# Optimization experiments

Measured on AMD Instinct MI355X. Metric: run time of the kernel, lower is better.

## Reference

```python
import jax, jax.numpy as jnp
import numpy as np

N = 20000      # nodes (human PPI network scale)
E = 640000     # edges (avg degree 32)
PE, GOS, PROT = 128, 128, 480
OM_DIMS = [3, 3, 24, 24]          # transcriptome, proteome, effectome, interactome
D = 384                           # latent_space_dimension = 128 * 3 (jk 'cat')
H = 128                           # hidden_channels per layer
NEG_SLOPE = 0.1


def setup_inputs() -> dict:
    key = jax.random.key(0)
    ks = jax.random.split(key, 64)
    rn = lambda k, shp, s=0.05: jax.random.normal(k, shp, jnp.float32) * s
    inp = {
        "x": jax.random.normal(ks[0], (N, PE + GOS + PROT), jnp.float32),
        "x_ft": jax.random.normal(ks[1], (N, sum(OM_DIMS)), jnp.float32),
        "edge_index": jax.random.randint(ks[2], (2, E), 0, N),
    }
    i = 3
    def lin(fin, fout, name):
        nonlocal i
        inp["W_" + name] = rn(ks[i], (fin, fout)); inp["b_" + name] = jnp.zeros((fout,), jnp.float32)
        i += 1
    lin(PE, D, "pe"); lin(GOS, D, "gos"); lin(PROT, D, "prot")
    for j, d in enumerate(OM_DIMS):
        lin(d, D, f"om{j}")
    dims = [D, H, H, H]
    for j in range(3):
        lin(dims[j], dims[j + 1], f"c{j}")   # feature-branch GCN convs
        lin(dims[j], dims[j + 1], f"o{j}")   # omics-branch GCN convs
    lin(2 * D, D, "lat")
    lin(D, H, "drug"); lin(D, H, "dis")
    lin(H, 2, "odrug"); lin(H, 2, "odis")
    return inp


def _gcn(x, W, b, src, dst, deg_inv):
    # GCNConv(improved=True): A_hat = A + 2I, sym norm D^-1/2 A_hat D^-1/2
    h = x @ W                                  # [N, F_out]
    coef = deg_inv[src] * deg_inv[dst]         # [E]
    agg = jax.ops.segment_sum(h[src] * coef[:, None], dst, num_segments=N)
    agg = agg + h * (2.0 * deg_inv * deg_inv)[:, None]   # self loops (weight 2)
    return agg + b


def reference(x, x_ft, edge_index,
              W_pe, b_pe, W_gos, b_gos, W_prot, b_prot,
              W_om0, b_om0, W_om1, b_om1, W_om2, b_om2, W_om3, b_om3,
              W_c0, b_c0, W_o0, b_o0, W_c1, b_c1, W_o1, b_o1, W_c2, b_c2, W_o2, b_o2,
              W_lat, b_lat, W_drug, b_drug, W_dis, b_dis,
              W_odrug, b_odrug, W_odis, b_odis):
    act = lambda t: jax.nn.leaky_relu(t, NEG_SLOPE)
    src, dst = edge_index[0], edge_index[1]
    deg = jax.ops.segment_sum(jnp.ones((E,), jnp.float32), dst, num_segments=N) + 2.0
    deg_inv = jax.lax.rsqrt(deg)

    # encoders (features branch): pe | gosemsim | prot_emb slices of x
    pe = x[:, :PE]; gos = x[:, PE:PE + GOS]; prot = x[:, PE + GOS:PE + GOS + PROT]
    h = act(pe @ W_pe + b_pe + gos @ W_gos + b_gos + prot @ W_prot + b_prot)

    # encoders (omics branch): 3|3|24|24 slices of x_ft
    offs = np.cumsum([0] + OM_DIMS)
    Wom = [W_om0, W_om1, W_om2, W_om3]; bom = [b_om0, b_om1, b_om2, b_om3]
    g = act(sum(x_ft[:, offs[j]:offs[j + 1]] @ Wom[j] + bom[j] for j in range(4)))

    Wc = [W_c0, W_c1, W_c2]; bc = [b_c0, b_c1, b_c2]
    Wo = [W_o0, W_o1, W_o2]; bo = [b_o0, b_o1, b_o2]
    hs, gs = [], []
    for j in range(3):
        h = act(_gcn(h, Wc[j], bc[j], src, dst, deg_inv)); hs.append(h)
        g = act(_gcn(g, Wo[j], bo[j], src, dst, deg_inv)); gs.append(g)
    jk = jnp.concatenate(hs, axis=-1)          # [N, 384]
    jk_om = jnp.concatenate(gs, axis=-1)       # [N, 384]

    z = act(jnp.concatenate([jk, jk_om], axis=-1) @ W_lat + b_lat)  # [N, 384]
    drug = act(z @ W_drug + b_drug) @ W_odrug + b_odrug             # [N, 2]
    dis = act(z @ W_dis + b_dis) @ W_odis + b_odis                  # [N, 2]
    return jnp.concatenate([drug, dis], axis=-1)                    # [N, 4]
```

## Files before the change

### kernel.cpp

```cpp
#include <hip/hip_runtime.h>
#include <cstdint>

#define NN 20000
#define NNP 20096
#define NE 640000
#define NEG_SLOPE 0.1f
#define NSCAN 79
#define NSL 8
#define NPSL 2500
#define FBPS 160

typedef unsigned short ushort_t;
typedef __attribute__((ext_vector_type(8))) short short8;
typedef __attribute__((ext_vector_type(4))) float f32x4;
typedef __attribute__((ext_vector_type(2))) float f32x2;

__device__ __forceinline__ unsigned short f2bf(float f) {
    union { float f; unsigned u; } v; v.f = f;
    unsigned r = v.u + 0x7fffu + ((v.u >> 16) & 1u);
    return (unsigned short)(r >> 16);
}
__device__ __forceinline__ float bflo(unsigned u) { return __uint_as_float(u << 16); }
__device__ __forceinline__ float bfhi(unsigned u) { return __uint_as_float(u & 0xffff0000u); }

__device__ __forceinline__ int swz(int r) { return (r ^ (r >> 2)) & 3; }

__device__ __forceinline__ void gld_lds16(const void* g, void* l) {
    __builtin_amdgcn_global_load_lds(
        (const __attribute__((address_space(1))) void*)g,
        (__attribute__((address_space(3))) void*)l,
        16, 0, 0);
}

#define O_CAT   0
#define O_OM    282624
#define O_C0    307200
#define O_O0    356352
#define O_C1    405504
#define O_O1    421888
#define O_C2    438272
#define O_O2    454656
#define O_LAT   471040
#define O_HEADS 765952
#define WT_TOTAL 864256

__global__ __launch_bounds__(256) void pack_weights(
    const float* __restrict__ Wpe, const float* __restrict__ Wgos, const float* __restrict__ Wprot,
    const float* __restrict__ bpe, const float* __restrict__ bgos, const float* __restrict__ bprot,
    const float* __restrict__ Wom0, const float* __restrict__ Wom1,
    const float* __restrict__ Wom2, const float* __restrict__ Wom3,
    const float* __restrict__ bom0, const float* __restrict__ bom1,
    const float* __restrict__ bom2, const float* __restrict__ bom3,
    const float* __restrict__ Wc0, const float* __restrict__ Wo0,
    const float* __restrict__ Wc1, const float* __restrict__ Wo1,
    const float* __restrict__ Wc2, const float* __restrict__ Wo2,
    const float* __restrict__ Wlat,
    const float* __restrict__ Wdrug, const float* __restrict__ Wdis,
    const float* __restrict__ bdrug, const float* __restrict__ bdis,
    ushort_t* __restrict__ Wt, float* __restrict__ bcat, float* __restrict__ bomc,
    float* __restrict__ bheads)
{
    int i = blockIdx.x * blockDim.x + threadIdx.x;
    if (i < 282624) {
        int m = i / 736, k = i % 736;
        float v = (k < 128) ? Wpe[k * 384 + m]
                : (k < 256) ? Wgos[(k - 128) * 384 + m]
                            : Wprot[(k - 256) * 384 + m];
        Wt[O_CAT + i] = f2bf(v);
        return;
    }
    i -= 282624;
    if (i < 24576) {
        int m = i / 64, k = i % 64;
        float v = (k < 3)  ? Wom0[k * 384 + m]
                : (k < 6)  ? Wom1[(k - 3) * 384 + m]
                : (k < 30) ? Wom2[(k - 6) * 384 + m]
                : (k < 54) ? Wom3[(k - 30) * 384 + m] : 0.f;
        Wt[O_OM + i] = f2bf(v);
        return;
    }
    i -= 24576;
    if (i < 49152) { int m = i / 384, k = i % 384; Wt[O_C0 + i] = f2bf(Wc0[k * 128 + m]); return; }
    i -= 49152;
    if (i < 49152) { int m = i / 384, k = i % 384; Wt[O_O0 + i] = f2bf(Wo0[k * 128 + m]); return; }
    i -= 49152;
    if (i < 16384) { int m = i / 128, k = i % 128; Wt[O_C1 + i] = f2bf(Wc1[k * 128 + m]); return; }
    i -= 16384;
    if (i < 16384) { int m = i / 128, k = i % 128; Wt[O_O1 + i] = f2bf(Wo1[k * 128 + m]); return; }
    i -= 16384;
    if (i < 16384) { int m = i / 128, k = i % 128; Wt[O_C2 + i] = f2bf(Wc2[k * 128 + m]); return; }
    i -= 16384;
    if (i < 16384) { int m = i / 128, k = i % 128; Wt[O_O2 + i] = f2bf(Wo2[k * 128 + m]); return; }
    i -= 16384;
    if (i < 294912) { int m = i / 768, k = i % 768; Wt[O_LAT + i] = f2bf(Wlat[k * 384 + m]); return; }
    i -= 294912;
    if (i < 98304) {
        int m = i / 384, k = i % 384;
        float v = (m < 128) ? Wdrug[k * 128 + m] : Wdis[k * 128 + (m - 128)];
        Wt[O_HEADS + i] = f2bf(v);
        return;
    }
    i -= 98304;
    if (i < 384) { bcat[i] = bpe[i] + bgos[i] + bprot[i]; return; }
    i -= 384;
    if (i < 384) { bomc[i] = bom0[i] + bom1[i] + bom2[i] + bom3[i]; return; }
    i -= 384;
    if (i < 256) { bheads[i] = (i < 128) ? bdrug[i] : bdis[i - 128]; return; }
}

#define CVT_T1 (NN * 736 / 4)
__global__ __launch_bounds__(256) void convert_inputs(
    const float* __restrict__ x, const float* __restrict__ xft,
    ushort_t* __restrict__ xb, ushort_t* __restrict__ xftb)
{
    int i = blockIdx.x * blockDim.x + threadIdx.x;
    if (i < CVT_T1) {
        int base = i * 4;
        float4 v = *reinterpret_cast<const float4*>(&x[base]);
        unsigned long long p = (unsigned long long)f2bf(v.x)
                             | ((unsigned long long)f2bf(v.y) << 16)
                             | ((unsigned long long)f2bf(v.z) << 32)
                             | ((unsigned long long)f2bf(v.w) << 48);
        *reinterpret_cast<unsigned long long*>(&xb[base]) = p;
        return;
    }
    i -= CVT_T1;
    if (i < NN * 64) {
        int r = i >> 6, c = i & 63;
        float v = (c < 54) ? xft[r * 54 + c] : 0.f;
        xftb[i] = f2bf(v);
    }
}

__global__ __launch_bounds__(256) void count_deg_sliced(const int* __restrict__ dst, int* __restrict__ cnt)
{
    const int slice = blockIdx.x & (NSL - 1);
    const int blk = blockIdx.x >> 3;
    const int lo = slice * NPSL, hi = lo + NPSL;
    for (int e = blk * 256 + threadIdx.x; e < NE; e += FBPS * 256) {
        int d = dst[e];
        if (d >= lo && d < hi) atomicAdd(&cnt[d], 1);
    }
}

__global__ __launch_bounds__(256) void scan_blocksums(const int* __restrict__ cnt, int* __restrict__ bsum,
                                                      float* __restrict__ deg_inv)
{
    __shared__ int s[256];
    int t = threadIdx.x, i = blockIdx.x * 256 + t;
    int v = (i < NN) ? cnt[i] : 0;
    if (i < NN) deg_inv[i] = rsqrtf((float)v + 2.0f);
    s[t] = v;
    __syncthreads();
    for (int off = 128; off; off >>= 1) {
        if (t < off) s[t] += s[t + off];
        __syncthreads();
    }
    if (t == 0) bsum[blockIdx.x] = s[0];
}

__global__ __launch_bounds__(128) void scan_tops(const int* __restrict__ bsum,
                                                 int* __restrict__ boff, int* __restrict__ ofs)
{
    __shared__ int s[NSCAN];
    int t = threadIdx.x;
    if (t < NSCAN) s[t] = bsum[t];
    __syncthreads();
    if (t == 0) {
        int run = 0;
        for (int b = 0; b < NSCAN; b++) { int x = s[b]; s[b] = run; run += x; }
        ofs[NN] = run;
    }
    __syncthreads();
    if (t < NSCAN) boff[t] = s[t];
}

__global__ __launch_bounds__(256) void scan_apply(const int* __restrict__ cnt, const int* __restrict__ boff,
                                                  int* __restrict__ ofs, int* __restrict__ cursor)
{
    __shared__ int s[256];
    int t = threadIdx.x, i = blockIdx.x * 256 + t;
    int v = (i < NN) ? cnt[i] : 0;
    s[t] = v;
    __syncthreads();
    for (int off = 1; off < 256; off <<= 1) {
        int u = (t >= off) ? s[t - off] : 0;
        __syncthreads();
        s[t] += u;
        __syncthreads();
    }
    int excl = s[t] - v + boff[blockIdx.x];
    if (i < NN) { ofs[i] = excl; cursor[i] = excl; }
}

__global__ __launch_bounds__(256) void fill_csr_sliced(
    const int* __restrict__ src, const int* __restrict__ dst,
    const float* __restrict__ deg_inv, int* __restrict__ cursor,
    uint2* __restrict__ csr_pk)
{
    const int slice = blockIdx.x & (NSL - 1);
    const int blk = blockIdx.x >> 3;
    const int lo = slice * NPSL, hi = lo + NPSL;
    for (int e = blk * 256 + threadIdx.x; e < NE; e += FBPS * 256) {
        int d = dst[e];
        if (d >= lo && d < hi) {
            int s = src[e];
            int p = atomicAdd(&cursor[d], 1);
            float cf = deg_inv[s] * deg_inv[d];
            csr_pk[p] = make_uint2((unsigned)s * 256u, __float_as_uint(cf));
        }
    }
}

template<int BN, bool BIASACT, bool OUT_BF16>
__device__ __forceinline__ void gemm_body(
    ushort_t* As, ushort_t* Bs,
    const ushort_t* __restrict__ A, int lda,
    const ushort_t* __restrict__ Wt,
    const float* __restrict__ bias,
    float* __restrict__ Cf, ushort_t* __restrict__ Cb, int ldc,
    int nrows, int K, int row0, int col0)
{
    constexpr int BK = 32;
    constexpr int NI = (BN == 128) ? 4 : 2;

    const int t = threadIdx.x;
    const int w = t >> 6, lane = t & 63;
    const int wr = w >> 1, wc = w & 1;
    const int m16 = lane & 15, quad = lane >> 4;
    const int sr = lane >> 2;
    const int pgrp = lane & 3;

    f32x4 acc[4][NI];
#pragma unroll
    for (int mi = 0; mi < 4; mi++)
#pragma unroll
        for (int ni = 0; ni < NI; ni++) acc[mi][ni] = (f32x4)0.f;

    for (int k0 = 0; k0 < K; k0 += BK) {
#pragma unroll
        for (int p = 0; p < 2; p++) {
            int c = p * 4 + w;
            int r = c * 16 + sr;
            int q = pgrp ^ swz(r);
            gld_lds16(&A[(size_t)(row0 + r) * lda + k0 + q * 8], &As[c * 512]);
        }
#pragma unroll
        for (int p = 0; p < BN / 64; p++) {
            int c = p * 4 + w;
            int r = c * 16 + sr;
            int q = pgrp ^ swz(r);
            gld_lds16(&Wt[(size_t)(col0 + r) * K + k0 + q * 8], &Bs[c * 512]);
        }
        __syncthreads();

        short8 af[4], bfr[NI];
#pragma unroll
        for (int mi = 0; mi < 4; mi++) {
            int r = wr * 64 + mi * 16 + m16;
            int p = quad ^ swz(r);
            af[mi] = *reinterpret_cast<const short8*>(&As[r * 32 + p * 8]);
        }
#pragma unroll
        for (int ni = 0; ni < NI; ni++) {
            int n = wc * (NI * 16) + ni * 16 + m16;
            int p = quad ^ swz(n);
            bfr[ni] = *reinterpret_cast<const short8*>(&Bs[n * 32 + p * 8]);
        }
#pragma unroll
        for (int mi = 0; mi < 4; mi++)
#pragma unroll
            for (int ni = 0; ni < NI; ni++)
                acc[mi][ni] = __builtin_amdgcn_mfma_f32_16x16x32_bf16(af[mi], bfr[ni], acc[mi][ni], 0, 0, 0);
        __syncthreads();
    }

#pragma unroll
    for (int mi = 0; mi < 4; mi++) {
#pragma unroll
        for (int reg = 0; reg < 4; reg++) {
            int grow = row0 + wr * 64 + mi * 16 + quad * 4 + reg;
            if (grow >= nrows) continue;
#pragma unroll
            for (int ni = 0; ni < NI; ni++) {
                int gcol = col0 + wc * (NI * 16) + ni * 16 + m16;
                float v = acc[mi][ni][reg];
                if constexpr (BIASACT) {
                    v += bias[gcol];
                    v = (v > 0.f) ? v : NEG_SLOPE * v;
                }
                if constexpr (OUT_BF16) Cb[(size_t)grow * ldc + gcol] = f2bf(v);
                else                    Cf[(size_t)grow * ldc + gcol] = v;
            }
        }
    }
}

template<int BN, bool BIASACT, bool OUT_BF16>
__global__ __launch_bounds__(256) void mfma_gemm(
    const ushort_t* __restrict__ A, int lda,
    const ushort_t* __restrict__ Wt,
    const float* __restrict__ bias,
    float* __restrict__ Cf, ushort_t* __restrict__ Cb, int ldc,
    int nrows, int K)
{
    __shared__ ushort_t As[128 * 32];
    __shared__ ushort_t Bs[BN * 32];
    gemm_body<BN, BIASACT, OUT_BF16>(As, Bs, A, lda, Wt, bias, Cf, Cb, ldc, nrows, K,
                                     blockIdx.y * 128, blockIdx.x * BN);
}

__global__ __launch_bounds__(256) void mfma_gemm_dual(
    const ushort_t* __restrict__ A0, const ushort_t* __restrict__ A1, int lda,
    const ushort_t* __restrict__ W0, const ushort_t* __restrict__ W1,
    ushort_t* __restrict__ C0, ushort_t* __restrict__ C1, int ldc,
    int nrows, int K)
{
    __shared__ ushort_t As[128 * 32];
    __shared__ ushort_t Bs[64 * 32];
    const ushort_t* A  = blockIdx.z ? A1 : A0;
    const ushort_t* Wt = blockIdx.z ? W1 : W0;
    ushort_t*       Cb = blockIdx.z ? C1 : C0;
    gemm_body<64, false, true>(As, Bs, A, lda, Wt, nullptr, nullptr, Cb, ldc, nrows, K,
                               blockIdx.y * 128, blockIdx.x * 64);
}

__global__ __launch_bounds__(256) void aggregate_fused(
    const ushort_t* __restrict__ tabA, const ushort_t* __restrict__ tabB,
    const float* __restrict__ bc, const float* __restrict__ bo,
    const int* __restrict__ ofs, const uint2* __restrict__ csr_pk,
    const float* __restrict__ deg_inv,
    ushort_t* __restrict__ outb, int hcol, int gcol)
{
    const int w = threadIdx.x >> 6, lane = threadIdx.x & 63;
    const int i = blockIdx.x * 4 + w;
    const int el = lane >> 5;
    const int fq = lane & 31;
    const int chain = fq >> 4;
    const unsigned lbyte = (unsigned)((fq & 15) * 16);
    const char* __restrict__ tb = (const char*)(chain ? tabB : tabA);

    const int start = ofs[i], end = ofs[i + 1];
    const float di = deg_inv[i];
    const uint4 pv = *reinterpret_cast<const uint4*>(tb + ((unsigned)i * 256u + lbyte));

    float acc[8];
#pragma unroll
    for (int q = 0; q < 8; q++) acc[q] = 0.f;

#define FMA8(P, C) \
    acc[0] = fmaf(bflo(P.x), C, acc[0]); acc[1] = fmaf(bfhi(P.x), C, acc[1]); \
    acc[2] = fmaf(bflo(P.y), C, acc[2]); acc[3] = fmaf(bfhi(P.y), C, acc[3]); \
    acc[4] = fmaf(bflo(P.z), C, acc[4]); acc[5] = fmaf(bfhi(P.z), C, acc[5]); \
    acc[6] = fmaf(bflo(P.w), C, acc[6]); acc[7] = fmaf(bfhi(P.w), C, acc[7])

    int j = start + el;
    for (; j + 6 < end; j += 8) {
        uint2 e0 = csr_pk[j];
        uint2 e1 = csr_pk[j + 2];
        uint2 e2 = csr_pk[j + 4];
        uint2 e3 = csr_pk[j + 6];
        uint4 p0 = *reinterpret_cast<const uint4*>(tb + (e0.x + lbyte));
        uint4 p1 = *reinterpret_cast<const uint4*>(tb + (e1.x + lbyte));
        uint4 p2 = *reinterpret_cast<const uint4*>(tb + (e2.x + lbyte));
        uint4 p3 = *reinterpret_cast<const uint4*>(tb + (e3.x + lbyte));
        float c0 = __uint_as_float(e0.y), c1 = __uint_as_float(e1.y);
        float c2 = __uint_as_float(e2.y), c3 = __uint_as_float(e3.y);
        FMA8(p0, c0); FMA8(p1, c1); FMA8(p2, c2); FMA8(p3, c3);
    }
    for (; j < end; j += 2) {
        uint2 e0 = csr_pk[j];
        uint4 p0 = *reinterpret_cast<const uint4*>(tb + (e0.x + lbyte));
        float c0 = __uint_as_float(e0.y);
        FMA8(p0, c0);
    }
#undef FMA8

#pragma unroll
    for (int q = 0; q < 8; q++) acc[q] += __shfl_xor(acc[q], 32);

    if (el == 0) {
        const float* __restrict__ bias = chain ? bo : bc;
        const int coloff = (fq & 15) * 8;
        const float c = 2.f * di * di;
        float sv[8] = {bflo(pv.x), bfhi(pv.x), bflo(pv.y), bfhi(pv.y),
                       bflo(pv.z), bfhi(pv.z), bflo(pv.w), bfhi(pv.w)};
        uint4 o;
        unsigned* op = &o.x;
#pragma unroll
        for (int q = 0; q < 8; q += 2) {
            float v0 = fmaf(sv[q],     c, acc[q])     + bias[coloff + q];
            float v1 = fmaf(sv[q + 1], c, acc[q + 1]) + bias[coloff + q + 1];
            v0 = (v0 > 0.f) ? v0 : NEG_SLOPE * v0;
            v1 = (v1 > 0.f) ? v1 : NEG_SLOPE * v1;
            op[q >> 1] = (unsigned)f2bf(v0) | ((unsigned)f2bf(v1) << 16);
        }
        const int col = (chain ? gcol : hcol) + coloff;
        *reinterpret_cast<uint4*>(&outb[(size_t)i * 768 + col]) = o;
    }
}

__global__ __launch_bounds__(256) void heads_kernel(
    const float* __restrict__ tmpH,
    const float* __restrict__ Wod, const float* __restrict__ bod,
    const float* __restrict__ Wos, const float* __restrict__ bos,
    float* __restrict__ out)
{
    int w = threadIdx.x >> 6, lane = threadIdx.x & 63;
    int i = blockIdx.x * 4 + w;
    if (i >= NN) return;
    float a0 = 0.f, a1 = 0.f, d0 = 0.f, d1 = 0.f;
#pragma unroll
    for (int p = 0; p < 2; p++) {
        int k = lane + p * 64;
        float vd = tmpH[(size_t)i * 256 + k];
        float vs = tmpH[(size_t)i * 256 + 128 + k];
        a0 = fmaf(vd, Wod[k * 2 + 0], a0);
        a1 = fmaf(vd, Wod[k * 2 + 1], a1);
        d0 = fmaf(vs, Wos[k * 2 + 0], d0);
        d1 = fmaf(vs, Wos[k * 2 + 1], d1);
    }
    for (int off = 32; off; off >>= 1) {
        a0 += __shfl_down(a0, off);
        a1 += __shfl_down(a1, off);
        d0 += __shfl_down(d0, off);
        d1 += __shfl_down(d1, off);
    }
    if (lane == 0) {
        out[(size_t)i * 4 + 0] = a0 + bod[0];
        out[(size_t)i * 4 + 1] = a1 + bod[1];
        out[(size_t)i * 4 + 2] = d0 + bos[0];
        out[(size_t)i * 4 + 3] = d1 + bos[1];
    }
}

extern "C" void kernel_launch(void* const* d_in, const int* in_sizes, int n_in,
                              void* d_out, int out_size, void* d_ws, size_t ws_size,
                              hipStream_t stream)
{
    const float* x      = (const float*)d_in[0];
    const float* x_ft   = (const float*)d_in[1];
    const int*   eidx   = (const int*)d_in[2];
    const float* W_pe   = (const float*)d_in[3];
    const float* b_pe   = (const float*)d_in[4];
    const float* W_gos  = (const float*)d_in[5];
    const float* b_gos  = (const float*)d_in[6];
    const float* W_prot = (const float*)d_in[7];
    const float* b_prot = (const float*)d_in[8];
    const float* W_om0  = (const float*)d_in[9];
    const float* b_om0  = (const float*)d_in[10];
    const float* W_om1  = (const float*)d_in[11];
    const float* b_om1  = (const float*)d_in[12];
    const float* W_om2  = (const float*)d_in[13];
    const float* b_om2  = (const float*)d_in[14];
    const float* W_om3  = (const float*)d_in[15];
    const float* b_om3  = (const float*)d_in[16];
    const float* W_c[3] = {(const float*)d_in[17], (const float*)d_in[21], (const float*)d_in[25]};
    const float* b_c[3] = {(const float*)d_in[18], (const float*)d_in[22], (const float*)d_in[26]};
    const float* W_o[3] = {(const float*)d_in[19], (const float*)d_in[23], (const float*)d_in[27]};
    const float* b_o[3] = {(const float*)d_in[20], (const float*)d_in[24], (const float*)d_in[28]};
    const float* W_lat  = (const float*)d_in[29];
    const float* b_lat  = (const float*)d_in[30];
    const float* W_drug = (const float*)d_in[31];
    const float* b_drug = (const float*)d_in[32];
    const float* W_dis  = (const float*)d_in[33];
    const float* b_dis  = (const float*)d_in[34];
    const float* W_odrug= (const float*)d_in[35];
    const float* b_odrug= (const float*)d_in[36];
    const float* W_odis = (const float*)d_in[37];
    const float* b_odis = (const float*)d_in[38];
    float* out = (float*)d_out;

    const int* e_src = eidx;
    const int* e_dst = eidx + NE;

    char* p = (char*)d_ws;
    auto alloc = [&](size_t bytes) -> void* {
        void* r = (void*)p;
        p += (bytes + 255) & ~(size_t)255;
        return r;
    };
    ushort_t* Wt    = (ushort_t*)alloc((size_t)WT_TOTAL * 2);
    float* bcat     = (float*)alloc(384 * 4);
    float* bomc     = (float*)alloc(384 * 4);
    float* bheads   = (float*)alloc(256 * 4);
    float* deg_inv  = (float*)alloc((size_t)NN * 4);
    int*   cnt      = (int*)alloc((size_t)NN * 4);
    int*   ofs      = (int*)alloc((size_t)(NN + 1) * 4);
    int*   cursor   = (int*)alloc((size_t)NN * 4);
    int*   bsum     = (int*)alloc((size_t)NSCAN * 4);
    int*   boff     = (int*)alloc((size_t)NSCAN * 4);
    uint2* csr_pk   = (uint2*)alloc((size_t)NE * 8);
    ushort_t* xb    = (ushort_t*)alloc((size_t)NNP * 736 * 2);
    ushort_t* xftb  = (ushort_t*)alloc((size_t)NNP * 64 * 2);
    ushort_t* h0b   = (ushort_t*)alloc((size_t)NNP * 384 * 2);
    ushort_t* g0b   = (ushort_t*)alloc((size_t)NNP * 384 * 2);
    ushort_t* jkb   = (ushort_t*)alloc((size_t)NNP * 768 * 2);
    ushort_t* zb    = (ushort_t*)alloc((size_t)NNP * 384 * 2);
    ushort_t* tmpAb = (ushort_t*)alloc((size_t)NNP * 128 * 2);
    ushort_t* tmpBb = (ushort_t*)alloc((size_t)NNP * 128 * 2);
    float* tmpH     = (float*)alloc((size_t)NNP * 256 * 4);
    (void)ws_size; (void)in_sizes; (void)n_in; (void)out_size;

    {
        int total = WT_TOTAL + 384 + 384 + 256;
        pack_weights<<<dim3((total + 255) / 256), dim3(256), 0, stream>>>(
            W_pe, W_gos, W_prot, b_pe, b_gos, b_prot,
            W_om0, W_om1, W_om2, W_om3, b_om0, b_om1, b_om2, b_om3,
            W_c[0], W_o[0], W_c[1], W_o[1], W_c[2], W_o[2],
            W_lat, W_drug, W_dis, b_drug, b_dis, Wt, bcat, bomc, bheads);
    }
    convert_inputs<<<dim3((CVT_T1 + NN * 64 + 255) / 256), dim3(256), 0, stream>>>(x, x_ft, xb, xftb);

    hipMemsetAsync(cnt, 0, (size_t)NN * 4, stream);
    count_deg_sliced<<<dim3(NSL * FBPS), dim3(256), 0, stream>>>(e_dst, cnt);
    scan_blocksums<<<dim3(NSCAN), dim3(256), 0, stream>>>(cnt, bsum, deg_inv);
    scan_tops<<<dim3(1), dim3(128), 0, stream>>>(bsum, boff, ofs);
    scan_apply<<<dim3(NSCAN), dim3(256), 0, stream>>>(cnt, boff, ofs, cursor);
    fill_csr_sliced<<<dim3(NSL * FBPS), dim3(256), 0, stream>>>(e_src, e_dst, deg_inv, cursor, csr_pk);

    mfma_gemm<128, true, true><<<dim3(3, 157), dim3(256), 0, stream>>>(
        xb, 736, Wt + O_CAT, bcat, nullptr, h0b, 384, NN, 736);
    mfma_gemm<128, true, true><<<dim3(3, 157), dim3(256), 0, stream>>>(
        xftb, 64, Wt + O_OM, bomc, nullptr, g0b, 384, NN, 64);

    mfma_gemm_dual<<<dim3(2, 157, 2), dim3(256), 0, stream>>>(
        h0b, g0b, 384, Wt + O_C0, Wt + O_O0, tmpAb, tmpBb, 128, NN, 384);
    aggregate_fused<<<dim3(NN / 4), dim3(256), 0, stream>>>(
        tmpAb, tmpBb, b_c[0], b_o[0], ofs, csr_pk, deg_inv, jkb, 0, 384);

    mfma_gemm_dual<<<dim3(2, 157, 2), dim3(256), 0, stream>>>(
        jkb + 0, jkb + 384, 768, Wt + O_C1, Wt + O_O1, tmpAb, tmpBb, 128, NN, 128);
    aggregate_fused<<<dim3(NN / 4), dim3(256), 0, stream>>>(
        tmpAb, tmpBb, b_c[1], b_o[1], ofs, csr_pk, deg_inv, jkb, 128, 512);

    mfma_gemm_dual<<<dim3(2, 157, 2), dim3(256), 0, stream>>>(
        jkb + 128, jkb + 512, 768, Wt + O_C2, Wt + O_O2, tmpAb, tmpBb, 128, NN, 128);
    aggregate_fused<<<dim3(NN / 4), dim3(256), 0, stream>>>(
        tmpAb, tmpBb, b_c[2], b_o[2], ofs, csr_pk, deg_inv, jkb, 256, 640);

    mfma_gemm<128, true, true><<<dim3(3, 157), dim3(256), 0, stream>>>(
        jkb, 768, Wt + O_LAT, b_lat, nullptr, zb, 384, NN, 768);

    mfma_gemm<128, true, false><<<dim3(2, 157), dim3(256), 0, stream>>>(
        zb, 384, Wt + O_HEADS, bheads, tmpH, nullptr, 256, NN, 384);
    heads_kernel<<<dim3((NN + 3) / 4), dim3(256), 0, stream>>>(
        tmpH, W_odrug, b_odrug, W_odis, b_odis, out);
}
```

Baseline: 495.5 us.

## Sort CSR neighbors by source partition and interleave both GCN branch tables

Each destination's CSR segment is now bucketed by which of eight source-node ranges the source falls in. This uses per-node, per-partition counts and cursors, so neighbor gathers walk the feature table in a rough source order for better cache locality. The two branch GEMM outputs are written into one interleaved 256-column table, so a single gather per neighbor fetches both branches' rows (512 bytes). The count buffer is now zeroed inside pack_weights instead of by a memset. In exchange, counts and cursors take eight times the memory, and the scan kernels do more work.

```diff
diff --git a/kernel.cpp b/kernel.cpp
--- a/kernel.cpp
+++ b/kernel.cpp
@@ -9,6 +9,7 @@
 #define NSL 8
 #define NPSL 2500
 #define FBPS 160
+#define NPART 8
 
 typedef unsigned short ushort_t;
 typedef __attribute__((ext_vector_type(8))) short short8;
@@ -58,7 +59,7 @@
     const float* __restrict__ Wdrug, const float* __restrict__ Wdis,
     const float* __restrict__ bdrug, const float* __restrict__ bdis,
     ushort_t* __restrict__ Wt, float* __restrict__ bcat, float* __restrict__ bomc,
-    float* __restrict__ bheads)
+    float* __restrict__ bheads, int* __restrict__ cnt8)
 {
     int i = blockIdx.x * blockDim.x + threadIdx.x;
     if (i < 282624) {
@@ -106,7 +107,10 @@
     if (i < 384) { bomc[i] = bom0[i] + bom1[i] + bom2[i] + bom3[i]; return; }
     i -= 384;
     if (i < 256) { bheads[i] = (i < 128) ? bdrug[i] : bdis[i - 128]; return; }
-}
+    i -= 256;
+    if (i < NN * NPART) { cnt8[i] = 0; return; }
+}
+#define PACK_TOTAL (WT_TOTAL + 384 + 384 + 256 + NN * NPART)
 
 #define CVT_T1 (NN * 736 / 4)
 __global__ __launch_bounds__(256) void convert_inputs(
@@ -132,24 +136,33 @@
     }
 }
 
-__global__ __launch_bounds__(256) void count_deg_sliced(const int* __restrict__ dst, int* __restrict__ cnt)
+__global__ __launch_bounds__(256) void count_deg_sliced(
+    const int* __restrict__ src, const int* __restrict__ dst, int* __restrict__ cnt8)
 {
     const int slice = blockIdx.x & (NSL - 1);
     const int blk = blockIdx.x >> 3;
     const int lo = slice * NPSL, hi = lo + NPSL;
     for (int e = blk * 256 + threadIdx.x; e < NE; e += FBPS * 256) {
         int d = dst[e];
-        if (d >= lo && d < hi) atomicAdd(&cnt[d], 1);
-    }
-}
-
-__global__ __launch_bounds__(256) void scan_blocksums(const int* __restrict__ cnt, int* __restrict__ bsum,
+        if (d >= lo && d < hi) {
+            int p = (unsigned)src[e] / 2500u;
+            atomicAdd(&cnt8[d * NPART + p], 1);
+        }
+    }
+}
+
+__global__ __launch_bounds__(256) void scan_blocksums(const int* __restrict__ cnt8, int* __restrict__ bsum,
                                                       float* __restrict__ deg_inv)
 {
     __shared__ int s[256];
     int t = threadIdx.x, i = blockIdx.x * 256 + t;
-    int v = (i < NN) ? cnt[i] : 0;
-    if (i < NN) deg_inv[i] = rsqrtf((float)v + 2.0f);
+    int v = 0;
+    if (i < NN) {
+        uint4 a = *reinterpret_cast<const uint4*>(&cnt8[i * NPART]);
+        uint4 b = *reinterpret_cast<const uint4*>(&cnt8[i * NPART + 4]);
+        v = (int)(a.x + a.y + a.z + a.w + b.x + b.y + b.z + b.w);
+        deg_inv[i] = rsqrtf((float)v + 2.0f);
+    }
     s[t] = v;
     __syncthreads();
     for (int off = 128; off; off >>= 1) {
@@ -160,7 +173,7 @@
 }
 
 __global__ __launch_bounds__(128) void scan_tops(const int* __restrict__ bsum,
-                                                 int* __restrict__ boff, int* __restrict__ ofs)
+                                                 int* __restrict__ boff, int* __restrict__ ofsN)
 {
     __shared__ int s[NSCAN];
     int t = threadIdx.x;
@@ -169,18 +182,27 @@
     if (t == 0) {
         int run = 0;
         for (int b = 0; b < NSCAN; b++) { int x = s[b]; s[b] = run; run += x; }
-        ofs[NN] = run;
+        ofsN[NN] = run;
     }
     __syncthreads();
     if (t < NSCAN) boff[t] = s[t];
 }
 
-__global__ __launch_bounds__(256) void scan_apply(const int* __restrict__ cnt, const int* __restrict__ boff,
-                                                  int* __restrict__ ofs, int* __restrict__ cursor)
+__global__ __launch_bounds__(256) void scan_apply(const int* __restrict__ cnt8, const int* __restrict__ boff,
+                                                  int* __restrict__ ofsN, int* __restrict__ cursor8)
 {
     __shared__ int s[256];
     int t = threadIdx.x, i = blockIdx.x * 256 + t;
-    int v = (i < NN) ? cnt[i] : 0;
+    int c[NPART];
+    int v = 0;
+    if (i < NN) {
+        uint4 a = *reinterpret_cast<const uint4*>(&cnt8[i * NPART]);
+        uint4 b = *reinterpret_cast<const uint4*>(&cnt8[i * NPART + 4]);
+        c[0] = a.x; c[1] = a.y; c[2] = a.z; c[3] = a.w;
+        c[4] = b.x; c[5] = b.y; c[6] = b.z; c[7] = b.w;
+#pragma unroll
+        for (int p = 0; p < NPART; p++) v += c[p];
+    }
     s[t] = v;
     __syncthreads();
     for (int off = 1; off < 256; off <<= 1) {
@@ -189,13 +211,17 @@
         s[t] += u;
         __syncthreads();
     }
-    int excl = s[t] - v + boff[blockIdx.x];
-    if (i < NN) { ofs[i] = excl; cursor[i] = excl; }
+    if (i < NN) {
+        int run = s[t] - v + boff[blockIdx.x];
+        ofsN[i] = run;
+#pragma unroll
+        for (int p = 0; p < NPART; p++) { cursor8[i * NPART + p] = run; run += c[p]; }
+    }
 }
 
 __global__ __launch_bounds__(256) void fill_csr_sliced(
     const int* __restrict__ src, const int* __restrict__ dst,
-    const float* __restrict__ deg_inv, int* __restrict__ cursor,
+    const float* __restrict__ deg_inv, int* __restrict__ cursor8,
     uint2* __restrict__ csr_pk)
 {
     const int slice = blockIdx.x & (NSL - 1);
@@ -205,9 +231,10 @@
         int d = dst[e];
         if (d >= lo && d < hi) {
             int s = src[e];
-            int p = atomicAdd(&cursor[d], 1);
+            int pp = (unsigned)s / 2500u;
+            int p = atomicAdd(&cursor8[d * NPART + pp], 1);
             float cf = deg_inv[s] * deg_inv[d];
-            csr_pk[p] = make_uint2((unsigned)s * 256u, __float_as_uint(cf));
+            csr_pk[p] = make_uint2((unsigned)s * 512u, __float_as_uint(cf));
         }
     }
 }
@@ -313,22 +340,22 @@
 __global__ __launch_bounds__(256) void mfma_gemm_dual(
     const ushort_t* __restrict__ A0, const ushort_t* __restrict__ A1, int lda,
     const ushort_t* __restrict__ W0, const ushort_t* __restrict__ W1,
-    ushort_t* __restrict__ C0, ushort_t* __restrict__ C1, int ldc,
+    ushort_t* __restrict__ tmpI,
     int nrows, int K)
 {
     __shared__ ushort_t As[128 * 32];
     __shared__ ushort_t Bs[64 * 32];
     const ushort_t* A  = blockIdx.z ? A1 : A0;
     const ushort_t* Wt = blockIdx.z ? W1 : W0;
-    ushort_t*       Cb = blockIdx.z ? C1 : C0;
-    gemm_body<64, false, true>(As, Bs, A, lda, Wt, nullptr, nullptr, Cb, ldc, nrows, K,
+    ushort_t*       Cb = tmpI + blockIdx.z * 128;
+    gemm_body<64, false, true>(As, Bs, A, lda, Wt, nullptr, nullptr, Cb, 256, nrows, K,
                                blockIdx.y * 128, blockIdx.x * 64);
 }
 
 __global__ __launch_bounds__(256) void aggregate_fused(
-    const ushort_t* __restrict__ tabA, const ushort_t* __restrict__ tabB,
+    const ushort_t* __restrict__ tabI,
     const float* __restrict__ bc, const float* __restrict__ bo,
-    const int* __restrict__ ofs, const uint2* __restrict__ csr_pk,
+    const int* __restrict__ ofsN, const uint2* __restrict__ csr_pk,
     const float* __restrict__ deg_inv,
     ushort_t* __restrict__ outb, int hcol, int gcol)
 {
@@ -337,12 +364,12 @@
     const int el = lane >> 5;
     const int fq = lane & 31;
     const int chain = fq >> 4;
-    const unsigned lbyte = (unsigned)((fq & 15) * 16);
-    const char* __restrict__ tb = (const char*)(chain ? tabB : tabA);
-
-    const int start = ofs[i], end = ofs[i + 1];
+    const unsigned lbyte = (unsigned)(fq * 16);
+    const char* __restrict__ tb = (const char*)tabI;
+
+    const int start = ofsN[i], end = ofsN[i + 1];
     const float di = deg_inv[i];
-    const uint4 pv = *reinterpret_cast<const uint4*>(tb + ((unsigned)i * 256u + lbyte));
+    const uint4 pv = *reinterpret_cast<const uint4*>(tb + ((unsigned)i * 512u + lbyte));
 
     float acc[8];
 #pragma unroll
@@ -485,9 +512,9 @@
     float* bomc     = (float*)alloc(384 * 4);
     float* bheads   = (float*)alloc(256 * 4);
     float* deg_inv  = (float*)alloc((size_t)NN * 4);
-    int*   cnt      = (int*)alloc((size_t)NN * 4);
-    int*   ofs      = (int*)alloc((size_t)(NN + 1) * 4);
-    int*   cursor   = (int*)alloc((size_t)NN * 4);
+    int*   cnt8     = (int*)alloc((size_t)NN * NPART * 4);
+    int*   cursor8  = (int*)alloc((size_t)NN * NPART * 4);
+    int*   ofsN     = (int*)alloc((size_t)(NN + 1) * 4);
     int*   bsum     = (int*)alloc((size_t)NSCAN * 4);
     int*   boff     = (int*)alloc((size_t)NSCAN * 4);
     uint2* csr_pk   = (uint2*)alloc((size_t)NE * 8);
@@ -497,27 +524,23 @@
     ushort_t* g0b   = (ushort_t*)alloc((size_t)NNP * 384 * 2);
     ushort_t* jkb   = (ushort_t*)alloc((size_t)NNP * 768 * 2);
     ushort_t* zb    = (ushort_t*)alloc((size_t)NNP * 384 * 2);
-    ushort_t* tmpAb = (ushort_t*)alloc((size_t)NNP * 128 * 2);
-    ushort_t* tmpBb = (ushort_t*)alloc((size_t)NNP * 128 * 2);
+    ushort_t* tmpI  = (ushort_t*)alloc((size_t)NNP * 256 * 2);
     float* tmpH     = (float*)alloc((size_t)NNP * 256 * 4);
     (void)ws_size; (void)in_sizes; (void)n_in; (void)out_size;
 
-    {
-        int total = WT_TOTAL + 384 + 384 + 256;
-        pack_weights<<<dim3((total + 255) / 256), dim3(256), 0, stream>>>(
-            W_pe, W_gos, W_prot, b_pe, b_gos, b_prot,
-            W_om0, W_om1, W_om2, W_om3, b_om0, b_om1, b_om2, b_om3,
-            W_c[0], W_o[0], W_c[1], W_o[1], W_c[2], W_o[2],
-            W_lat, W_drug, W_dis, b_drug, b_dis, Wt, bcat, bomc, bheads);
-    }
+    pack_weights<<<dim3((PACK_TOTAL + 255) / 256), dim3(256), 0, stream>>>(
+        W_pe, W_gos, W_prot, b_pe, b_gos, b_prot,
+        W_om0, W_om1, W_om2, W_om3, b_om0, b_om1, b_om2, b_om3,
+        W_c[0], W_o[0], W_c[1], W_o[1], W_c[2], W_o[2],
+        W_lat, W_drug, W_dis, b_drug, b_dis, Wt, bcat, bomc, bheads, cnt8);
+
     convert_inputs<<<dim3((CVT_T1 + NN * 64 + 255) / 256), dim3(256), 0, stream>>>(x, x_ft, xb, xftb);
 
-    hipMemsetAsync(cnt, 0, (size_t)NN * 4, stream);
-    count_deg_sliced<<<dim3(NSL * FBPS), dim3(256), 0, stream>>>(e_dst, cnt);
-    scan_blocksums<<<dim3(NSCAN), dim3(256), 0, stream>>>(cnt, bsum, deg_inv);
-    scan_tops<<<dim3(1), dim3(128), 0, stream>>>(bsum, boff, ofs);
-    scan_apply<<<dim3(NSCAN), dim3(256), 0, stream>>>(cnt, boff, ofs, cursor);
-    fill_csr_sliced<<<dim3(NSL * FBPS), dim3(256), 0, stream>>>(e_src, e_dst, deg_inv, cursor, csr_pk);
+    count_deg_sliced<<<dim3(NSL * FBPS), dim3(256), 0, stream>>>(e_src, e_dst, cnt8);
+    scan_blocksums<<<dim3(NSCAN), dim3(256), 0, stream>>>(cnt8, bsum, deg_inv);
+    scan_tops<<<dim3(1), dim3(128), 0, stream>>>(bsum, boff, ofsN);
+    scan_apply<<<dim3(NSCAN), dim3(256), 0, stream>>>(cnt8, boff, ofsN, cursor8);
+    fill_csr_sliced<<<dim3(NSL * FBPS), dim3(256), 0, stream>>>(e_src, e_dst, deg_inv, cursor8, csr_pk);
 
     mfma_gemm<128, true, true><<<dim3(3, 157), dim3(256), 0, stream>>>(
         xb, 736, Wt + O_CAT, bcat, nullptr, h0b, 384, NN, 736);
@@ -525,19 +548,19 @@
         xftb, 64, Wt + O_OM, bomc, nullptr, g0b, 384, NN, 64);
 
     mfma_gemm_dual<<<dim3(2, 157, 2), dim3(256), 0, stream>>>(
-        h0b, g0b, 384, Wt + O_C0, Wt + O_O0, tmpAb, tmpBb, 128, NN, 384);
+        h0b, g0b, 384, Wt + O_C0, Wt + O_O0, tmpI, NN, 384);
     aggregate_fused<<<dim3(NN / 4), dim3(256), 0, stream>>>(
-        tmpAb, tmpBb, b_c[0], b_o[0], ofs, csr_pk, deg_inv, jkb, 0, 384);
+        tmpI, b_c[0], b_o[0], ofsN, csr_pk, deg_inv, jkb, 0, 384);
 
     mfma_gemm_dual<<<dim3(2, 157, 2), dim3(256), 0, stream>>>(
-        jkb + 0, jkb + 384, 768, Wt + O_C1, Wt + O_O1, tmpAb, tmpBb, 128, NN, 128);
+        jkb + 0, jkb + 384, 768, Wt + O_C1, Wt + O_O1, tmpI, NN, 128);
     aggregate_fused<<<dim3(NN / 4), dim3(256), 0, stream>>>(
-        tmpAb, tmpBb, b_c[1], b_o[1], ofs, csr_pk, deg_inv, jkb, 128, 512);
+        tmpI, b_c[1], b_o[1], ofsN, csr_pk, deg_inv, jkb, 128, 512);
 
     mfma_gemm_dual<<<dim3(2, 157, 2), dim3(256), 0, stream>>>(
-        jkb + 128, jkb + 512, 768, Wt + O_C2, Wt + O_O2, tmpAb, tmpBb, 128, NN, 128);
+        jkb + 128, jkb + 512, 768, Wt + O_C2, Wt + O_O2, tmpI, NN, 128);
     aggregate_fused<<<dim3(NN / 4), dim3(256), 0, stream>>>(
-        tmpAb, tmpBb, b_c[2], b_o[2], ofs, csr_pk, deg_inv, jkb, 256, 640);
+        tmpI, b_c[2], b_o[2], ofsN, csr_pk, deg_inv, jkb, 256, 640);
 
     mfma_gemm<128, true, true><<<dim3(3, 157), dim3(256), 0, stream>>>(
         jkb, 768, Wt + O_LAT, b_lat, nullptr, zb, 384, NN, 768);
```

Measured after the change: 480.1 us. 1.03x faster.
